# Kernel optimization log

Hardware: AMD Instinct MI355X
Metric: run time of the kernel (lower is better)

The kernel has to match this reference:

```python
import jax, jax.numpy as jnp
import numpy as np

U, I, D, L = 100000, 50000, 64, 2
E_S, E_I = 1200000, 1200000

def spmm(rows, cols, vals, x, num_rows):
    # sparse A (COO) @ dense x : gather source rows, scale, segment-sum into dest rows
    return jax.ops.segment_sum(vals[:, None] * x[cols], rows, num_segments=num_rows)

def setup_inputs() -> dict:
    key = jax.random.key(0)
    ks = jax.random.split(key, 9)
    return {
        "user_emb": jax.random.normal(ks[0], (U, D), jnp.float32) * 0.1,
        "item_emb": jax.random.normal(ks[1], (I, D), jnp.float32) * 0.1,
        "weights": jax.random.normal(ks[2], (L, 2 * D, D), jnp.float32) * (1.0 / np.sqrt(2 * D)),
        "social_vals": jax.random.uniform(ks[3], (E_S,), jnp.float32),
        "inter_vals": jax.random.uniform(ks[4], (E_I,), jnp.float32),
        "social_rows": jax.random.randint(ks[5], (E_S,), 0, U, jnp.int32),
        "social_cols": jax.random.randint(ks[6], (E_S,), 0, U, jnp.int32),
        "inter_rows": jax.random.randint(ks[7], (E_I,), 0, U, jnp.int32),
        "inter_cols": jax.random.randint(ks[8], (E_I,), 0, I, jnp.int32),
    }

def reference(user_emb, item_emb, weights, social_vals, inter_vals,
              social_rows, social_cols, inter_rows, inter_cols):
    u = user_emb
    num_users = user_emb.shape[0]
    for k in range(weights.shape[0]):
        new_u = spmm(social_rows, social_cols, social_vals, u, num_users)  # [U, D]
        u = jnp.concatenate([new_u, u], axis=1) @ weights[k]               # [U, 2D] @ [2D, D]
    final_u = u + spmm(inter_rows, inter_cols, inter_vals, item_emb, num_users)
    return (final_u, item_emb)
```

## Files before the change

### kernel.cpp

```cpp
#include <hip/hip_runtime.h>

#define DD 64
#define RPCB 1024
#define CBSH 10
#define NBLK_P 256

static inline size_t align16(size_t x) { return (x + 15) & ~(size_t)15; }

__device__ __forceinline__ unsigned bf16rn(float f) {
    unsigned u = __float_as_uint(f);
    return (u + 0x7fffu + ((u >> 16) & 1u)) >> 16;
}

typedef __attribute__((ext_vector_type(8))) short bf16x8;
typedef __attribute__((ext_vector_type(4))) float f32x4;

#define VAL_SCALE 32767.0f
#define VAL_INV   (1.0f / 32767.0f)

__global__ __launch_bounds__(1024) void p1_hist(
    const int* __restrict__ srows, const int* __restrict__ irows,
    int* __restrict__ hmat, int ES, int EI, int U, int CB, int EPB)
{
    __shared__ int hist[256];
    const int b = blockIdx.x, t = threadIdx.x;
    for (int i = t; i < CB; i += 1024) hist[i] = 0;
    __syncthreads();
    const int e0 = b * EPB, e1 = min(e0 + EPB, ES + EI);
    for (int e = e0 + t; e < e1; e += 1024) {
        int row = (e < ES) ? srows[e] : U + irows[e - ES];
        atomicAdd(&hist[row >> CBSH], 1);
    }
    __syncthreads();
    for (int i = t; i < CB; i += 1024) hmat[(size_t)i * NBLK_P + b] = hist[i];
}

__global__ __launch_bounds__(256) void scan_partial(
    const int* __restrict__ in, int* __restrict__ out, int* __restrict__ bsums, int n)
{
    __shared__ int sh[256];
    int base = blockIdx.x * 2048 + threadIdx.x * 8;
    int v[8];
    int tsum = 0;
    #pragma unroll
    for (int j = 0; j < 8; ++j) {
        int idx = base + j;
        int x = (idx < n) ? in[idx] : 0;
        v[j] = tsum;
        tsum += x;
    }
    sh[threadIdx.x] = tsum;
    __syncthreads();
    for (int off = 1; off < 256; off <<= 1) {
        int t = (threadIdx.x >= off) ? sh[threadIdx.x - off] : 0;
        __syncthreads();
        sh[threadIdx.x] += t;
        __syncthreads();
    }
    int texc = sh[threadIdx.x] - tsum;
    #pragma unroll
    for (int j = 0; j < 8; ++j) {
        int idx = base + j;
        if (idx < n) out[idx] = texc + v[j];
    }
    if (threadIdx.x == 255) bsums[blockIdx.x] = sh[255];
}

__global__ void scan_top(int* bsums, int nb)
{
    int run = 0;
    for (int i = 0; i < nb; ++i) { int t = bsums[i]; bsums[i] = run; run += t; }
}

__global__ __launch_bounds__(256) void scan_add(
    int* __restrict__ out, const int* __restrict__ bsums, int n)
{
    int i = blockIdx.x * 256 + threadIdx.x;
    if (i < n) out[i] += bsums[i >> 11];
}

__global__ __launch_bounds__(1024) void p2_scatter(
    const int* __restrict__ srows, const int* __restrict__ scols, const float* __restrict__ svals,
    const int* __restrict__ irows, const int* __restrict__ icols, const float* __restrict__ ivals,
    const int* __restrict__ hS, uint2* __restrict__ bedges,
    int ES, int EI, int U, int CB, int EPB)
{
    __shared__ int cur[256];
    const int b = blockIdx.x, t = threadIdx.x;
    for (int i = t; i < CB; i += 1024) cur[i] = hS[(size_t)i * NBLK_P + b];
    __syncthreads();
    const int e0 = b * EPB, e1 = min(e0 + EPB, ES + EI);
    for (int e = e0 + t; e < e1; e += 1024) {
        int row, col; float val;
        if (e < ES) { row = srows[e]; col = scols[e]; val = svals[e]; }
        else {
            int i = e - ES;
            row = U + irows[i]; col = icols[i]; val = ivals[i];
        }
        unsigned q = (unsigned)(val * VAL_SCALE + 0.5f);
        int slot = atomicAdd(&cur[row >> CBSH], 1);
        bedges[slot] = make_uint2(((unsigned)(row & (RPCB - 1)) << 17) | (unsigned)col,
                                  (unsigned)col | (q << 17));
    }
}

__global__ __launch_bounds__(256) void p3_fin(
    const uint2* __restrict__ bedges, const int* __restrict__ hS,
    int* __restrict__ row_ptr, unsigned* __restrict__ edges,
    int n2, int Etot, int CB)
{
    __shared__ int cnt[RPCB];
    __shared__ int sh[256];
    const int cb = blockIdx.x, t = threadIdx.x;
    const int r0 = cb << CBSH;
    const int s = hS[(size_t)cb * NBLK_P];
    const int e = (cb == CB - 1) ? Etot : hS[(size_t)(cb + 1) * NBLK_P];

    #pragma unroll
    for (int j = 0; j < RPCB / 256; ++j) cnt[t + j * 256] = 0;
    __syncthreads();
    for (int i = s + t; i < e; i += 256) atomicAdd(&cnt[bedges[i].x >> 17], 1);
    __syncthreads();

    int c[4]; int tot = 0;
    #pragma unroll
    for (int j = 0; j < 4; ++j) { int x = cnt[t * 4 + j]; c[j] = tot; tot += x; }
    sh[t] = tot;
    __syncthreads();
    for (int off = 1; off < 256; off <<= 1) {
        int v = (t >= off) ? sh[t - off] : 0;
        __syncthreads();
        sh[t] += v;
        __syncthreads();
    }
    int excl = sh[t] - tot;
    #pragma unroll
    for (int j = 0; j < 4; ++j) {
        int r = t * 4 + j;
        int v = s + excl + c[j];
        cnt[r] = v;
        int gr = r0 + r;
        if (gr < n2) row_ptr[gr] = v;
    }
    if (cb == CB - 1 && t == 0) row_ptr[n2] = Etot;
    __syncthreads();

    for (int i = s + t; i < e; i += 256) {
        uint2 ev = bedges[i];
        int r = ev.x >> 17;
        int slot = atomicAdd(&cnt[r], 1);
        edges[slot] = ev.y;
    }
}

__global__ __launch_bounds__(256) void conv_quant(
    const float* __restrict__ uemb, ushort* __restrict__ ubf,
    unsigned char* __restrict__ uq8, float* __restrict__ uscale, int U,
    const float* __restrict__ iemb, unsigned char* __restrict__ iq8,
    float* __restrict__ iscale, float* __restrict__ passI, int I)
{
    int row  = (blockIdx.x * 256 + threadIdx.x) >> 3;
    int lane = threadIdx.x & 7;
    bool isU = (row < U);
    int lrow = isU ? row : row - U;
    if (!isU && lrow >= I) return;
    const float* src = (isU ? uemb : iemb) + ((size_t)lrow << 6) + lane * 8;
    float4 A = *reinterpret_cast<const float4*>(src);
    float4 B = *reinterpret_cast<const float4*>(src + 4);
    float m = fmaxf(fmaxf(fmaxf(fabsf(A.x), fabsf(A.y)), fmaxf(fabsf(A.z), fabsf(A.w))),
                    fmaxf(fmaxf(fabsf(B.x), fabsf(B.y)), fmaxf(fabsf(B.z), fabsf(B.w))));
    m = fmaxf(m, __shfl_xor(m, 1, 8));
    m = fmaxf(m, __shfl_xor(m, 2, 8));
    m = fmaxf(m, __shfl_xor(m, 4, 8));
    float inv = (m > 1e-30f) ? 127.0f / m : 0.0f;
    float sc  = m / 127.0f;
    unsigned b0 = (unsigned)(__float2int_rn(A.x * inv) + 128);
    unsigned b1 = (unsigned)(__float2int_rn(A.y * inv) + 128);
    unsigned b2 = (unsigned)(__float2int_rn(A.z * inv) + 128);
    unsigned b3 = (unsigned)(__float2int_rn(A.w * inv) + 128);
    unsigned b4 = (unsigned)(__float2int_rn(B.x * inv) + 128);
    unsigned b5 = (unsigned)(__float2int_rn(B.y * inv) + 128);
    unsigned b6 = (unsigned)(__float2int_rn(B.z * inv) + 128);
    unsigned b7 = (unsigned)(__float2int_rn(B.w * inv) + 128);
    uint2 pk = make_uint2(b0 | (b1 << 8) | (b2 << 16) | (b3 << 24),
                          b4 | (b5 << 8) | (b6 << 16) | (b7 << 24));
    if (isU) {
        reinterpret_cast<uint2*>(uq8 + ((size_t)lrow << 6) + lane * 8)[0] = pk;
        if (lane == 0) uscale[lrow] = sc;
        uint4 r;
        r.x = bf16rn(A.x) | (bf16rn(A.y) << 16);
        r.y = bf16rn(A.z) | (bf16rn(A.w) << 16);
        r.z = bf16rn(B.x) | (bf16rn(B.y) << 16);
        r.w = bf16rn(B.z) | (bf16rn(B.w) << 16);
        *reinterpret_cast<uint4*>(ubf + ((size_t)lrow << 6) + lane * 8) = r;
    } else {
        reinterpret_cast<uint2*>(iq8 + ((size_t)lrow << 6) + lane * 8)[0] = pk;
        if (lane == 0) iscale[lrow] = sc;
        float* q = passI + ((size_t)lrow << 6) + lane * 8;
        *reinterpret_cast<float4*>(q)     = A;
        *reinterpret_cast<float4*>(q + 4) = B;
    }
}

__global__ __launch_bounds__(256) void rows_to_i8(
    const ushort* __restrict__ bf, unsigned char* __restrict__ q8,
    float* __restrict__ scale, int nrows)
{
    int row  = (blockIdx.x * 256 + threadIdx.x) >> 3;
    int lane = threadIdx.x & 7;
    if (row >= nrows) return;
    uint4 x = *reinterpret_cast<const uint4*>(bf + ((size_t)row << 6) + lane * 8);
    float v0 = __uint_as_float(x.x << 16), v1 = __uint_as_float(x.x & 0xffff0000u);
    float v2 = __uint_as_float(x.y << 16), v3 = __uint_as_float(x.y & 0xffff0000u);
    float v4 = __uint_as_float(x.z << 16), v5 = __uint_as_float(x.z & 0xffff0000u);
    float v6 = __uint_as_float(x.w << 16), v7 = __uint_as_float(x.w & 0xffff0000u);
    float m = fmaxf(fmaxf(fmaxf(fabsf(v0), fabsf(v1)), fmaxf(fabsf(v2), fabsf(v3))),
                    fmaxf(fmaxf(fabsf(v4), fabsf(v5)), fmaxf(fabsf(v6), fabsf(v7))));
    m = fmaxf(m, __shfl_xor(m, 1, 8));
    m = fmaxf(m, __shfl_xor(m, 2, 8));
    m = fmaxf(m, __shfl_xor(m, 4, 8));
    float inv = (m > 1e-30f) ? 127.0f / m : 0.0f;
    unsigned b0 = (unsigned)(__float2int_rn(v0 * inv) + 128);
    unsigned b1 = (unsigned)(__float2int_rn(v1 * inv) + 128);
    unsigned b2 = (unsigned)(__float2int_rn(v2 * inv) + 128);
    unsigned b3 = (unsigned)(__float2int_rn(v3 * inv) + 128);
    unsigned b4 = (unsigned)(__float2int_rn(v4 * inv) + 128);
    unsigned b5 = (unsigned)(__float2int_rn(v5 * inv) + 128);
    unsigned b6 = (unsigned)(__float2int_rn(v6 * inv) + 128);
    unsigned b7 = (unsigned)(__float2int_rn(v7 * inv) + 128);
    uint2 pk = make_uint2(b0 | (b1 << 8) | (b2 << 16) | (b3 << 24),
                          b4 | (b5 << 8) | (b6 << 16) | (b7 << 24));
    reinterpret_cast<uint2*>(q8 + ((size_t)row << 6) + lane * 8)[0] = pk;
    if (lane == 0) scale[row] = m / 127.0f;
}

__global__ __launch_bounds__(256) void conv_w(
    const float* __restrict__ w, ushort* __restrict__ wtb, int n)
{
    int idx = blockIdx.x * 256 + threadIdx.x;
    if (idx >= n) return;
    int l = idx >> 13;
    int r = idx & 8191;
    int c = r >> 7;
    int k = r & 127;
    wtb[idx] = (ushort)bf16rn(w[(size_t)l * 8192 + k * 64 + c]);
}

__device__ __forceinline__ void fma_i8(float4& a0, float4& a1, float& ssum, float veff, uint2 x)
{
    ssum += veff;
    a0.x += veff * (float)(x.x & 0xffu);
    a0.y += veff * (float)((x.x >> 8) & 0xffu);
    a0.z += veff * (float)((x.x >> 16) & 0xffu);
    a0.w += veff * (float)(x.x >> 24);
    a1.x += veff * (float)(x.y & 0xffu);
    a1.y += veff * (float)((x.y >> 8) & 0xffu);
    a1.z += veff * (float)((x.y >> 16) & 0xffu);
    a1.w += veff * (float)(x.y >> 24);
}

template <int MODE>
__global__ __launch_bounds__(256) void spmm_i8(
    const int* __restrict__ row_ptr, const unsigned* __restrict__ edges,
    const unsigned char* __restrict__ q8,
    const float* __restrict__ scalef,
    ushort* __restrict__ outb, float* __restrict__ outf, int nrows)
{
    int g    = (blockIdx.x * 256 + threadIdx.x) >> 3;
    int lane = threadIdx.x & 7;
    if (g >= nrows) return;
    int s = row_ptr[g], e = row_ptr[g + 1];
    float4 a0 = make_float4(0.f, 0.f, 0.f, 0.f);
    float4 a1 = make_float4(0.f, 0.f, 0.f, 0.f);
    float ssum = 0.f;
    int i = s;
    for (; i + 3 < e; i += 4) {
        unsigned e0 = edges[i], e1 = edges[i + 1], e2 = edges[i + 2], e3 = edges[i + 3];
        unsigned c0 = e0 & 0x1FFFFu, c1 = e1 & 0x1FFFFu, c2 = e2 & 0x1FFFFu, c3 = e3 & 0x1FFFFu;
        uint2 x0 = *reinterpret_cast<const uint2*>(q8 + ((size_t)c0 << 6) + lane * 8);
        uint2 x1 = *reinterpret_cast<const uint2*>(q8 + ((size_t)c1 << 6) + lane * 8);
        uint2 x2 = *reinterpret_cast<const uint2*>(q8 + ((size_t)c2 << 6) + lane * 8);
        uint2 x3 = *reinterpret_cast<const uint2*>(q8 + ((size_t)c3 << 6) + lane * 8);
        float v0 = (float)(e0 >> 17) * VAL_INV * scalef[c0];
        float v1 = (float)(e1 >> 17) * VAL_INV * scalef[c1];
        float v2 = (float)(e2 >> 17) * VAL_INV * scalef[c2];
        float v3 = (float)(e3 >> 17) * VAL_INV * scalef[c3];
        fma_i8(a0, a1, ssum, v0, x0);
        fma_i8(a0, a1, ssum, v1, x1);
        fma_i8(a0, a1, ssum, v2, x2);
        fma_i8(a0, a1, ssum, v3, x3);
    }
    for (; i < e; ++i) {
        unsigned e0 = edges[i];
        unsigned c0 = e0 & 0x1FFFFu;
        uint2 x0 = *reinterpret_cast<const uint2*>(q8 + ((size_t)c0 << 6) + lane * 8);
        float v0 = (float)(e0 >> 17) * VAL_INV * scalef[c0];
        fma_i8(a0, a1, ssum, v0, x0);
    }
    float bias = 128.f * ssum;
    a0.x -= bias; a0.y -= bias; a0.z -= bias; a0.w -= bias;
    a1.x -= bias; a1.y -= bias; a1.z -= bias; a1.w -= bias;
    if (MODE == 0) {
        uint4 pk;
        pk.x = bf16rn(a0.x) | (bf16rn(a0.y) << 16);
        pk.y = bf16rn(a0.z) | (bf16rn(a0.w) << 16);
        pk.z = bf16rn(a1.x) | (bf16rn(a1.y) << 16);
        pk.w = bf16rn(a1.z) | (bf16rn(a1.w) << 16);
        *reinterpret_cast<uint4*>(outb + ((size_t)g << 6) + lane * 8) = pk;
    } else {
        float* o = outf + ((size_t)g << 6) + lane * 8;
        float4 c0 = *reinterpret_cast<const float4*>(o);
        float4 c1 = *reinterpret_cast<const float4*>(o + 4);
        a0.x += c0.x; a0.y += c0.y; a0.z += c0.z; a0.w += c0.w;
        a1.x += c1.x; a1.y += c1.y; a1.z += c1.z; a1.w += c1.w;
        *reinterpret_cast<float4*>(o)     = a0;
        *reinterpret_cast<float4*>(o + 4) = a1;
    }
}

template<bool FINAL>
__global__ __launch_bounds__(256) void gemm_mfma(
    const ushort* __restrict__ abf,
    const ushort* __restrict__ bbf,
    const ushort* __restrict__ wtb,
    float* __restrict__ outf,
    ushort* __restrict__ outb,
    int U)
{
    __shared__ ushort sWt[64 * 128];
    const int t = threadIdx.x;

    for (int i = t; i < 1024; i += 256) {
        int c = i >> 4, g = i & 15;
        uint4 v = *reinterpret_cast<const uint4*>(wtb + (size_t)c * 128 + g * 8);
        int gp = g ^ (c & 7);
        *reinterpret_cast<uint4*>(&sWt[c * 128 + gp * 8]) = v;
    }
    __syncthreads();

    const int w    = t >> 6;
    const int l    = t & 63;
    const int l16  = l & 15;
    const int ksub = l >> 4;
    const int grow_base = blockIdx.x * 64 + w * 16;

    const int arow = min(grow_base + l16, U - 1);

    f32x4 acc[4] = {f32x4{0,0,0,0}, f32x4{0,0,0,0}, f32x4{0,0,0,0}, f32x4{0,0,0,0}};

    #pragma unroll
    for (int kk = 0; kk < 4; ++kk) {
        const int kof = kk * 32 + ksub * 8;
        const ushort* asrc = (kk < 2) ? (abf + ((size_t)arow << 6) + kof)
                                      : (bbf + ((size_t)arow << 6) + (kof - 64));
        bf16x8 afrag = *reinterpret_cast<const bf16x8*>(asrc);
        #pragma unroll
        for (int ct = 0; ct < 4; ++ct) {
            int c  = ct * 16 + l16;
            int g  = kk * 4 + ksub;
            int gp = g ^ (c & 7);
            bf16x8 bfrag = *reinterpret_cast<const bf16x8*>(&sWt[c * 128 + gp * 8]);
            acc[ct] = __builtin_amdgcn_mfma_f32_16x16x32_bf16(afrag, bfrag, acc[ct], 0, 0, 0);
        }
    }

    #pragma unroll
    for (int ct = 0; ct < 4; ++ct) {
        #pragma unroll
        for (int j = 0; j < 4; ++j) {
            int grow = grow_base + ksub * 4 + j;
            int gcol = ct * 16 + l16;
            if (grow < U) {
                float v = acc[ct][j];
                if (FINAL) outf[((size_t)grow << 6) + gcol] = v;
                else       outb[((size_t)grow << 6) + gcol] = (ushort)bf16rn(v);
            }
        }
    }
}

extern "C" void kernel_launch(void* const* d_in, const int* in_sizes, int n_in,
                              void* d_out, int out_size, void* d_ws, size_t ws_size,
                              hipStream_t stream)
{
    const float* user_emb    = (const float*)d_in[0];
    const float* item_emb    = (const float*)d_in[1];
    const float* weights     = (const float*)d_in[2];
    const float* social_vals = (const float*)d_in[3];
    const float* inter_vals  = (const float*)d_in[4];
    const int*   social_rows = (const int*)d_in[5];
    const int*   social_cols = (const int*)d_in[6];
    const int*   inter_rows  = (const int*)d_in[7];
    const int*   inter_cols  = (const int*)d_in[8];

    const int D  = DD;
    const int U  = in_sizes[0] / D;
    const int I  = in_sizes[1] / D;
    const int L  = in_sizes[2] / (2 * D * D);
    const int ES = in_sizes[3];
    const int EI = in_sizes[4];

    float* out      = (float*)d_out;
    float* out_item = out + (size_t)U * D;

    char* p = (char*)d_ws;
    size_t off = 0;
    auto take = [&](size_t bytes) { char* r = p + off; off += align16(bytes); return r; };

    const int n2   = 2 * U;
    const int CB   = (n2 + RPCB - 1) >> CBSH;
    const int Etot = ES + EI;
    const int EPB  = (Etot + NBLK_P - 1) / NBLK_P;
    const int NH   = CB * NBLK_P;

    int*           row_ptr = (int*)take((size_t)(n2 + 1) * sizeof(int));
    int*           hmat    = (int*)take((size_t)NH * sizeof(int));
    int*           hS      = (int*)take((size_t)NH * sizeof(int));
    int*           bsums   = (int*)take(1024 * sizeof(int));
    unsigned*      edges   = (unsigned*)take((size_t)Etot * sizeof(unsigned));
    uint2*         bedges  = (uint2*)take((size_t)Etot * sizeof(uint2));
    ushort*        ubf     = (ushort*)take((size_t)U * D * sizeof(ushort));
    unsigned char* uq8     = (unsigned char*)take((size_t)U * D);
    float*         uscale  = (float*)take((size_t)U * sizeof(float));
    unsigned char* iq8     = (unsigned char*)take((size_t)I * D);
    float*         iscale  = (float*)take((size_t)I * sizeof(float));
    ushort*        wtb     = (ushort*)take((size_t)L * 2 * D * D * sizeof(ushort));
    ushort*        tmpA_bf = (ushort*)take((size_t)U * D * sizeof(ushort));
    ushort*        uB_bf   = (ushort*)take((size_t)U * D * sizeof(ushort));
    ushort*        uC_bf   = (ushort*)take((size_t)U * D * sizeof(ushort));
    unsigned char* uB_q8   = (unsigned char*)take((size_t)U * D);
    unsigned char* uC_q8   = (unsigned char*)take((size_t)U * D);
    float*         uB_sc   = (float*)take((size_t)U * sizeof(float));
    float*         uC_sc   = (float*)take((size_t)U * sizeof(float));

    p1_hist<<<NBLK_P, 1024, 0, stream>>>(social_rows, inter_rows, hmat, ES, EI, U, CB, EPB);
    const int nb = (NH + 2047) / 2048;
    scan_partial<<<nb, 256, 0, stream>>>(hmat, hS, bsums, NH);
    scan_top<<<1, 1, 0, stream>>>(bsums, nb);
    scan_add<<<(NH + 255) / 256, 256, 0, stream>>>(hS, bsums, NH);
    p2_scatter<<<NBLK_P, 1024, 0, stream>>>(
        social_rows, social_cols, social_vals,
        inter_rows, inter_cols, inter_vals,
        hS, bedges, ES, EI, U, CB, EPB);
    p3_fin<<<CB, 256, 0, stream>>>(bedges, hS, row_ptr, edges, n2, Etot, CB);

    const int convthreads = (U + I) * 8;
    conv_quant<<<(convthreads + 255) / 256, 256, 0, stream>>>(
        user_emb, ubf, uq8, uscale, U, item_emb, iq8, iscale, out_item, I);
    const int nw = L * 2 * D * D;
    conv_w<<<(nw + 255) / 256, 256, 0, stream>>>(weights, wtb, nw);

    const int spmm_grid = ((U * 8) + 255) / 256;
    const int gemm_grid = (U + 63) / 64;
    const ushort*        uprev_bf = ubf;
    const unsigned char* uprev_q8 = uq8;
    const float*         uprev_sc = uscale;
    int which = 0;
    for (int k = 0; k < L; ++k) {
        const ushort* wk = wtb + (size_t)k * 2 * D * D;
        spmm_i8<0><<<spmm_grid, 256, 0, stream>>>(
            row_ptr, edges, uprev_q8, uprev_sc, tmpA_bf, (float*)nullptr, U);
        if (k == L - 1) {
            gemm_mfma<true><<<gemm_grid, 256, 0, stream>>>(
                tmpA_bf, uprev_bf, wk, out, (ushort*)nullptr, U);
        } else {
            ushort*        nbf = which ? uC_bf : uB_bf;
            unsigned char* nq8 = which ? uC_q8 : uB_q8;
            float*         nsc = which ? uC_sc : uB_sc;
            gemm_mfma<false><<<gemm_grid, 256, 0, stream>>>(
                tmpA_bf, uprev_bf, wk, (float*)nullptr, nbf, U);
            rows_to_i8<<<spmm_grid, 256, 0, stream>>>(nbf, nq8, nsc, U);
            uprev_bf = nbf;
            uprev_q8 = nq8;
            uprev_sc = nsc;
            which ^= 1;
        }
    }

    spmm_i8<1><<<spmm_grid, 256, 0, stream>>>(
        row_ptr + U, edges, iq8, iscale, (ushort*)nullptr, out, U);
}
```

Baseline: 186.7 us.

## Fuse CSR build into cooperative kernel, merge conversions, fold int8 quantization into GEMM

Replaces the six-kernel CSR construction (histogram, three-stage scan, scatter, finalize) with a single cooperative kernel that uses grid-wide syncs between phases. The embedding and weight conversion kernels are merged into one launch. The int8 row quantization that ran as a separate pass after the intermediate GEMM now happens in that GEMM's epilogue through shared memory. The goal is to cut launch overhead and an extra round trip through global memory, at the cost of grid.sync barriers and the constraint that all 256 blocks of 1024 threads must be co-resident.

```diff
diff --git a/kernel.cpp b/kernel.cpp
--- a/kernel.cpp
+++ b/kernel.cpp
@@ -1,4 +1,7 @@
 #include <hip/hip_runtime.h>
+#include <hip/hip_cooperative_groups.h>
+
+namespace cg = cooperative_groups;
 
 #define DD 64
 #define RPCB 1024
@@ -18,232 +21,184 @@
 #define VAL_SCALE 32767.0f
 #define VAL_INV   (1.0f / 32767.0f)
 
-__global__ __launch_bounds__(1024) void p1_hist(
-    const int* __restrict__ srows, const int* __restrict__ irows,
-    int* __restrict__ hmat, int ES, int EI, int U, int CB, int EPB)
-{
-    __shared__ int hist[256];
+__global__ __launch_bounds__(1024) void build_csr_coop(
+    const int* __restrict__ srows, const int* __restrict__ scols, const float* __restrict__ svals,
+    const int* __restrict__ irows, const int* __restrict__ icols, const float* __restrict__ ivals,
+    int* __restrict__ hmat,
+    int* __restrict__ btot,
+    uint2* __restrict__ bedges,
+    int* __restrict__ row_ptr, unsigned* __restrict__ edges,
+    int ES, int EI, int U, int n2, int CB, int EPB)
+{
+    cg::grid_group grid = cg::this_grid();
     const int b = blockIdx.x, t = threadIdx.x;
-    for (int i = t; i < CB; i += 1024) hist[i] = 0;
+    const int Etot = ES + EI;
+    __shared__ int sh[1024];
+    __shared__ int sh2[256];
+
+    for (int i = t; i < CB; i += 1024) sh[i] = 0;
     __syncthreads();
-    const int e0 = b * EPB, e1 = min(e0 + EPB, ES + EI);
+    const int e0 = b * EPB, e1 = min(e0 + EPB, Etot);
     for (int e = e0 + t; e < e1; e += 1024) {
         int row = (e < ES) ? srows[e] : U + irows[e - ES];
-        atomicAdd(&hist[row >> CBSH], 1);
+        atomicAdd(&sh[row >> CBSH], 1);
     }
     __syncthreads();
-    for (int i = t; i < CB; i += 1024) hmat[(size_t)i * NBLK_P + b] = hist[i];
-}
-
-__global__ __launch_bounds__(256) void scan_partial(
-    const int* __restrict__ in, int* __restrict__ out, int* __restrict__ bsums, int n)
-{
-    __shared__ int sh[256];
-    int base = blockIdx.x * 2048 + threadIdx.x * 8;
-    int v[8];
-    int tsum = 0;
-    #pragma unroll
-    for (int j = 0; j < 8; ++j) {
-        int idx = base + j;
-        int x = (idx < n) ? in[idx] : 0;
-        v[j] = tsum;
-        tsum += x;
-    }
-    sh[threadIdx.x] = tsum;
+    for (int i = t; i < CB; i += 1024) hmat[(size_t)i * NBLK_P + b] = sh[i];
+    __threadfence();
+    grid.sync();
+
+    if (b < CB) {
+        int part = 0;
+        for (int i = t; i < NBLK_P; i += 1024) part += hmat[(size_t)b * NBLK_P + i];
+        sh[t] = part;
+        __syncthreads();
+        for (int off = 512; off > 0; off >>= 1) {
+            if (t < off) sh[t] += sh[t + off];
+            __syncthreads();
+        }
+        if (t == 0) btot[b] = sh[0];
+    }
+    __threadfence();
+    grid.sync();
+
+    if (b == 0) {
+        int v = (t < CB) ? btot[t] : 0;
+        if (t < 256) sh[t] = v;
+        __syncthreads();
+        for (int off = 1; off < 256; off <<= 1) {
+            int u2 = (t >= off && t < 256) ? sh[t - off] : 0;
+            __syncthreads();
+            if (t < 256) sh[t] += u2;
+            __syncthreads();
+        }
+        if (t < CB) btot[t] = sh[t] - v;
+    }
+    __threadfence();
+    grid.sync();
+
+    if (b < CB) {
+        int base = btot[b];
+        int v = (t < NBLK_P) ? hmat[(size_t)b * NBLK_P + t] : 0;
+        if (t < 256) sh[t] = v;
+        __syncthreads();
+        for (int off = 1; off < NBLK_P; off <<= 1) {
+            int u2 = (t >= off && t < 256) ? sh[t - off] : 0;
+            __syncthreads();
+            if (t < 256) sh[t] += u2;
+            __syncthreads();
+        }
+        if (t < NBLK_P) hmat[(size_t)b * NBLK_P + t] = base + sh[t] - v;
+    }
+    __threadfence();
+    grid.sync();
+
+    for (int i = t; i < CB; i += 1024) sh2[i] = hmat[(size_t)i * NBLK_P + b];
     __syncthreads();
-    for (int off = 1; off < 256; off <<= 1) {
-        int t = (threadIdx.x >= off) ? sh[threadIdx.x - off] : 0;
-        __syncthreads();
-        sh[threadIdx.x] += t;
-        __syncthreads();
-    }
-    int texc = sh[threadIdx.x] - tsum;
-    #pragma unroll
-    for (int j = 0; j < 8; ++j) {
-        int idx = base + j;
-        if (idx < n) out[idx] = texc + v[j];
-    }
-    if (threadIdx.x == 255) bsums[blockIdx.x] = sh[255];
-}
-
-__global__ void scan_top(int* bsums, int nb)
-{
-    int run = 0;
-    for (int i = 0; i < nb; ++i) { int t = bsums[i]; bsums[i] = run; run += t; }
-}
-
-__global__ __launch_bounds__(256) void scan_add(
-    int* __restrict__ out, const int* __restrict__ bsums, int n)
-{
-    int i = blockIdx.x * 256 + threadIdx.x;
-    if (i < n) out[i] += bsums[i >> 11];
-}
-
-__global__ __launch_bounds__(1024) void p2_scatter(
-    const int* __restrict__ srows, const int* __restrict__ scols, const float* __restrict__ svals,
-    const int* __restrict__ irows, const int* __restrict__ icols, const float* __restrict__ ivals,
-    const int* __restrict__ hS, uint2* __restrict__ bedges,
-    int ES, int EI, int U, int CB, int EPB)
-{
-    __shared__ int cur[256];
-    const int b = blockIdx.x, t = threadIdx.x;
-    for (int i = t; i < CB; i += 1024) cur[i] = hS[(size_t)i * NBLK_P + b];
-    __syncthreads();
-    const int e0 = b * EPB, e1 = min(e0 + EPB, ES + EI);
     for (int e = e0 + t; e < e1; e += 1024) {
         int row, col; float val;
         if (e < ES) { row = srows[e]; col = scols[e]; val = svals[e]; }
-        else {
-            int i = e - ES;
-            row = U + irows[i]; col = icols[i]; val = ivals[i];
-        }
+        else { int i = e - ES; row = U + irows[i]; col = icols[i]; val = ivals[i]; }
         unsigned q = (unsigned)(val * VAL_SCALE + 0.5f);
-        int slot = atomicAdd(&cur[row >> CBSH], 1);
+        int slot = atomicAdd(&sh2[row >> CBSH], 1);
         bedges[slot] = make_uint2(((unsigned)(row & (RPCB - 1)) << 17) | (unsigned)col,
                                   (unsigned)col | (q << 17));
     }
-}
-
-__global__ __launch_bounds__(256) void p3_fin(
-    const uint2* __restrict__ bedges, const int* __restrict__ hS,
-    int* __restrict__ row_ptr, unsigned* __restrict__ edges,
-    int n2, int Etot, int CB)
-{
-    __shared__ int cnt[RPCB];
-    __shared__ int sh[256];
-    const int cb = blockIdx.x, t = threadIdx.x;
-    const int r0 = cb << CBSH;
-    const int s = hS[(size_t)cb * NBLK_P];
-    const int e = (cb == CB - 1) ? Etot : hS[(size_t)(cb + 1) * NBLK_P];
-
-    #pragma unroll
-    for (int j = 0; j < RPCB / 256; ++j) cnt[t + j * 256] = 0;
-    __syncthreads();
-    for (int i = s + t; i < e; i += 256) atomicAdd(&cnt[bedges[i].x >> 17], 1);
-    __syncthreads();
-
-    int c[4]; int tot = 0;
-    #pragma unroll
-    for (int j = 0; j < 4; ++j) { int x = cnt[t * 4 + j]; c[j] = tot; tot += x; }
-    sh[t] = tot;
-    __syncthreads();
-    for (int off = 1; off < 256; off <<= 1) {
-        int v = (t >= off) ? sh[t - off] : 0;
-        __syncthreads();
-        sh[t] += v;
-        __syncthreads();
-    }
-    int excl = sh[t] - tot;
-    #pragma unroll
-    for (int j = 0; j < 4; ++j) {
-        int r = t * 4 + j;
-        int v = s + excl + c[j];
-        cnt[r] = v;
-        int gr = r0 + r;
+    __threadfence();
+    grid.sync();
+
+    if (b < CB) {
+        const int r0 = b << CBSH;
+        const int s = hmat[(size_t)b * NBLK_P];
+        const int e = (b == CB - 1) ? Etot : hmat[(size_t)(b + 1) * NBLK_P];
+        sh[t] = 0;
+        __syncthreads();
+        for (int i = s + t; i < e; i += 1024) atomicAdd(&sh[bedges[i].x >> 17], 1);
+        __syncthreads();
+        int c = sh[t];
+        __syncthreads();
+        sh[t] = c;
+        __syncthreads();
+        for (int off = 1; off < 1024; off <<= 1) {
+            int u2 = (t >= off) ? sh[t - off] : 0;
+            __syncthreads();
+            sh[t] += u2;
+            __syncthreads();
+        }
+        int v = s + sh[t] - c;
+        __syncthreads();
+        sh[t] = v;
+        int gr = r0 + t;
         if (gr < n2) row_ptr[gr] = v;
-    }
-    if (cb == CB - 1 && t == 0) row_ptr[n2] = Etot;
-    __syncthreads();
-
-    for (int i = s + t; i < e; i += 256) {
-        uint2 ev = bedges[i];
-        int r = ev.x >> 17;
-        int slot = atomicAdd(&cnt[r], 1);
-        edges[slot] = ev.y;
-    }
-}
-
-__global__ __launch_bounds__(256) void conv_quant(
+        if (b == CB - 1 && t == 0) row_ptr[n2] = Etot;
+        __syncthreads();
+        for (int i = s + t; i < e; i += 1024) {
+            uint2 ev = bedges[i];
+            int slot = atomicAdd(&sh[ev.x >> 17], 1);
+            edges[slot] = ev.y;
+        }
+    }
+}
+
+__global__ __launch_bounds__(256) void conv_all(
     const float* __restrict__ uemb, ushort* __restrict__ ubf,
     unsigned char* __restrict__ uq8, float* __restrict__ uscale, int U,
     const float* __restrict__ iemb, unsigned char* __restrict__ iq8,
-    float* __restrict__ iscale, float* __restrict__ passI, int I)
-{
-    int row  = (blockIdx.x * 256 + threadIdx.x) >> 3;
-    int lane = threadIdx.x & 7;
-    bool isU = (row < U);
-    int lrow = isU ? row : row - U;
-    if (!isU && lrow >= I) return;
-    const float* src = (isU ? uemb : iemb) + ((size_t)lrow << 6) + lane * 8;
-    float4 A = *reinterpret_cast<const float4*>(src);
-    float4 B = *reinterpret_cast<const float4*>(src + 4);
-    float m = fmaxf(fmaxf(fmaxf(fabsf(A.x), fabsf(A.y)), fmaxf(fabsf(A.z), fabsf(A.w))),
-                    fmaxf(fmaxf(fabsf(B.x), fabsf(B.y)), fmaxf(fabsf(B.z), fabsf(B.w))));
-    m = fmaxf(m, __shfl_xor(m, 1, 8));
-    m = fmaxf(m, __shfl_xor(m, 2, 8));
-    m = fmaxf(m, __shfl_xor(m, 4, 8));
-    float inv = (m > 1e-30f) ? 127.0f / m : 0.0f;
-    float sc  = m / 127.0f;
-    unsigned b0 = (unsigned)(__float2int_rn(A.x * inv) + 128);
-    unsigned b1 = (unsigned)(__float2int_rn(A.y * inv) + 128);
-    unsigned b2 = (unsigned)(__float2int_rn(A.z * inv) + 128);
-    unsigned b3 = (unsigned)(__float2int_rn(A.w * inv) + 128);
-    unsigned b4 = (unsigned)(__float2int_rn(B.x * inv) + 128);
-    unsigned b5 = (unsigned)(__float2int_rn(B.y * inv) + 128);
-    unsigned b6 = (unsigned)(__float2int_rn(B.z * inv) + 128);
-    unsigned b7 = (unsigned)(__float2int_rn(B.w * inv) + 128);
-    uint2 pk = make_uint2(b0 | (b1 << 8) | (b2 << 16) | (b3 << 24),
-                          b4 | (b5 << 8) | (b6 << 16) | (b7 << 24));
-    if (isU) {
-        reinterpret_cast<uint2*>(uq8 + ((size_t)lrow << 6) + lane * 8)[0] = pk;
-        if (lane == 0) uscale[lrow] = sc;
-        uint4 r;
-        r.x = bf16rn(A.x) | (bf16rn(A.y) << 16);
-        r.y = bf16rn(A.z) | (bf16rn(A.w) << 16);
-        r.z = bf16rn(B.x) | (bf16rn(B.y) << 16);
-        r.w = bf16rn(B.z) | (bf16rn(B.w) << 16);
-        *reinterpret_cast<uint4*>(ubf + ((size_t)lrow << 6) + lane * 8) = r;
+    float* __restrict__ iscale, float* __restrict__ passI, int I,
+    const float* __restrict__ w, ushort* __restrict__ wtb, int nw)
+{
+    int idx = blockIdx.x * 256 + threadIdx.x;
+    const int qthreads = (U + I) * 8;
+    if (idx < qthreads) {
+        int row  = idx >> 3;
+        int lane = idx & 7;
+        bool isU = (row < U);
+        int lrow = isU ? row : row - U;
+        const float* src = (isU ? uemb : iemb) + ((size_t)lrow << 6) + lane * 8;
+        float4 A = *reinterpret_cast<const float4*>(src);
+        float4 B = *reinterpret_cast<const float4*>(src + 4);
+        float m = fmaxf(fmaxf(fmaxf(fabsf(A.x), fabsf(A.y)), fmaxf(fabsf(A.z), fabsf(A.w))),
+                        fmaxf(fmaxf(fabsf(B.x), fabsf(B.y)), fmaxf(fabsf(B.z), fabsf(B.w))));
+        m = fmaxf(m, __shfl_xor(m, 1, 8));
+        m = fmaxf(m, __shfl_xor(m, 2, 8));
+        m = fmaxf(m, __shfl_xor(m, 4, 8));
+        float inv = (m > 1e-30f) ? 127.0f / m : 0.0f;
+        unsigned b0 = (unsigned)(__float2int_rn(A.x * inv) + 128);
+        unsigned b1 = (unsigned)(__float2int_rn(A.y * inv) + 128);
+        unsigned b2 = (unsigned)(__float2int_rn(A.z * inv) + 128);
+        unsigned b3 = (unsigned)(__float2int_rn(A.w * inv) + 128);
+        unsigned b4 = (unsigned)(__float2int_rn(B.x * inv) + 128);
+        unsigned b5 = (unsigned)(__float2int_rn(B.y * inv) + 128);
+        unsigned b6 = (unsigned)(__float2int_rn(B.z * inv) + 128);
+        unsigned b7 = (unsigned)(__float2int_rn(B.w * inv) + 128);
+        uint2 pk = make_uint2(b0 | (b1 << 8) | (b2 << 16) | (b3 << 24),
+                              b4 | (b5 << 8) | (b6 << 16) | (b7 << 24));
+        if (isU) {
+            reinterpret_cast<uint2*>(uq8 + ((size_t)lrow << 6) + lane * 8)[0] = pk;
+            if (lane == 0) uscale[lrow] = m / 127.0f;
+            uint4 r;
+            r.x = bf16rn(A.x) | (bf16rn(A.y) << 16);
+            r.y = bf16rn(A.z) | (bf16rn(A.w) << 16);
+            r.z = bf16rn(B.x) | (bf16rn(B.y) << 16);
+            r.w = bf16rn(B.z) | (bf16rn(B.w) << 16);
+            *reinterpret_cast<uint4*>(ubf + ((size_t)lrow << 6) + lane * 8) = r;
+        } else {
+            reinterpret_cast<uint2*>(iq8 + ((size_t)lrow << 6) + lane * 8)[0] = pk;
+            if (lane == 0) iscale[lrow] = m / 127.0f;
+            float* q = passI + ((size_t)lrow << 6) + lane * 8;
+            *reinterpret_cast<float4*>(q)     = A;
+            *reinterpret_cast<float4*>(q + 4) = B;
+        }
     } else {
-        reinterpret_cast<uint2*>(iq8 + ((size_t)lrow << 6) + lane * 8)[0] = pk;
-        if (lane == 0) iscale[lrow] = sc;
-        float* q = passI + ((size_t)lrow << 6) + lane * 8;
-        *reinterpret_cast<float4*>(q)     = A;
-        *reinterpret_cast<float4*>(q + 4) = B;
-    }
-}
-
-__global__ __launch_bounds__(256) void rows_to_i8(
-    const ushort* __restrict__ bf, unsigned char* __restrict__ q8,
-    float* __restrict__ scale, int nrows)
-{
-    int row  = (blockIdx.x * 256 + threadIdx.x) >> 3;
-    int lane = threadIdx.x & 7;
-    if (row >= nrows) return;
-    uint4 x = *reinterpret_cast<const uint4*>(bf + ((size_t)row << 6) + lane * 8);
-    float v0 = __uint_as_float(x.x << 16), v1 = __uint_as_float(x.x & 0xffff0000u);
-    float v2 = __uint_as_float(x.y << 16), v3 = __uint_as_float(x.y & 0xffff0000u);
-    float v4 = __uint_as_float(x.z << 16), v5 = __uint_as_float(x.z & 0xffff0000u);
-    float v6 = __uint_as_float(x.w << 16), v7 = __uint_as_float(x.w & 0xffff0000u);
-    float m = fmaxf(fmaxf(fmaxf(fabsf(v0), fabsf(v1)), fmaxf(fabsf(v2), fabsf(v3))),
-                    fmaxf(fmaxf(fabsf(v4), fabsf(v5)), fmaxf(fabsf(v6), fabsf(v7))));
-    m = fmaxf(m, __shfl_xor(m, 1, 8));
-    m = fmaxf(m, __shfl_xor(m, 2, 8));
-    m = fmaxf(m, __shfl_xor(m, 4, 8));
-    float inv = (m > 1e-30f) ? 127.0f / m : 0.0f;
-    unsigned b0 = (unsigned)(__float2int_rn(v0 * inv) + 128);
-    unsigned b1 = (unsigned)(__float2int_rn(v1 * inv) + 128);
-    unsigned b2 = (unsigned)(__float2int_rn(v2 * inv) + 128);
-    unsigned b3 = (unsigned)(__float2int_rn(v3 * inv) + 128);
-    unsigned b4 = (unsigned)(__float2int_rn(v4 * inv) + 128);
-    unsigned b5 = (unsigned)(__float2int_rn(v5 * inv) + 128);
-    unsigned b6 = (unsigned)(__float2int_rn(v6 * inv) + 128);
-    unsigned b7 = (unsigned)(__float2int_rn(v7 * inv) + 128);
-    uint2 pk = make_uint2(b0 | (b1 << 8) | (b2 << 16) | (b3 << 24),
-                          b4 | (b5 << 8) | (b6 << 16) | (b7 << 24));
-    reinterpret_cast<uint2*>(q8 + ((size_t)row << 6) + lane * 8)[0] = pk;
-    if (lane == 0) scale[row] = m / 127.0f;
-}
-
-__global__ __launch_bounds__(256) void conv_w(
-    const float* __restrict__ w, ushort* __restrict__ wtb, int n)
-{
-    int idx = blockIdx.x * 256 + threadIdx.x;
-    if (idx >= n) return;
-    int l = idx >> 13;
-    int r = idx & 8191;
-    int c = r >> 7;
-    int k = r & 127;
-    wtb[idx] = (ushort)bf16rn(w[(size_t)l * 8192 + k * 64 + c]);
+        int widx = idx - qthreads;
+        if (widx < nw) {
+            int l = widx >> 13;
+            int r = widx & 8191;
+            int c = r >> 7;
+            int k = r & 127;
+            wtb[widx] = (ushort)bf16rn(w[(size_t)l * 8192 + k * 64 + c]);
+        }
+    }
 }
 
 __device__ __forceinline__ void fma_i8(float4& a0, float4& a1, float& ssum, float veff, uint2 x)
@@ -325,6 +280,8 @@
     const ushort* __restrict__ wtb,
     float* __restrict__ outf,
     ushort* __restrict__ outb,
+    unsigned char* __restrict__ q8,
+    float* __restrict__ scale,
     int U)
 {
     __shared__ ushort sWt[64 * 128];
@@ -343,7 +300,6 @@
     const int l16  = l & 15;
     const int ksub = l >> 4;
     const int grow_base = blockIdx.x * 64 + w * 16;
-
     const int arow = min(grow_base + l16, U - 1);
 
     f32x4 acc[4] = {f32x4{0,0,0,0}, f32x4{0,0,0,0}, f32x4{0,0,0,0}, f32x4{0,0,0,0}};
@@ -364,16 +320,59 @@
         }
     }
 
-    #pragma unroll
-    for (int ct = 0; ct < 4; ++ct) {
+    if (FINAL) {
         #pragma unroll
-        for (int j = 0; j < 4; ++j) {
-            int grow = grow_base + ksub * 4 + j;
-            int gcol = ct * 16 + l16;
+        for (int ct = 0; ct < 4; ++ct) {
+            #pragma unroll
+            for (int j = 0; j < 4; ++j) {
+                int grow = grow_base + ksub * 4 + j;
+                int gcol = ct * 16 + l16;
+                if (grow < U) outf[((size_t)grow << 6) + gcol] = acc[ct][j];
+            }
+        }
+    } else {
+        __syncthreads();
+        ushort* sOut = sWt;
+        #pragma unroll
+        for (int ct = 0; ct < 4; ++ct) {
+            #pragma unroll
+            for (int j = 0; j < 4; ++j) {
+                int rloc = w * 16 + ksub * 4 + j;
+                int col  = ct * 16 + l16;
+                sOut[rloc * 72 + col] = (ushort)bf16rn(acc[ct][j]);
+            }
+        }
+        __syncthreads();
+        #pragma unroll
+        for (int pass = 0; pass < 2; ++pass) {
+            int rloc = pass * 32 + (t >> 3);
+            int lane = t & 7;
+            int grow = blockIdx.x * 64 + rloc;
+            uint4 x = *reinterpret_cast<const uint4*>(&sOut[rloc * 72 + lane * 8]);
+            float v0 = __uint_as_float(x.x << 16), v1 = __uint_as_float(x.x & 0xffff0000u);
+            float v2 = __uint_as_float(x.y << 16), v3 = __uint_as_float(x.y & 0xffff0000u);
+            float v4 = __uint_as_float(x.z << 16), v5 = __uint_as_float(x.z & 0xffff0000u);
+            float v6 = __uint_as_float(x.w << 16), v7 = __uint_as_float(x.w & 0xffff0000u);
+            float m = fmaxf(fmaxf(fmaxf(fabsf(v0), fabsf(v1)), fmaxf(fabsf(v2), fabsf(v3))),
+                            fmaxf(fmaxf(fabsf(v4), fabsf(v5)), fmaxf(fabsf(v6), fabsf(v7))));
+            m = fmaxf(m, __shfl_xor(m, 1, 8));
+            m = fmaxf(m, __shfl_xor(m, 2, 8));
+            m = fmaxf(m, __shfl_xor(m, 4, 8));
+            float inv = (m > 1e-30f) ? 127.0f / m : 0.0f;
+            unsigned b0 = (unsigned)(__float2int_rn(v0 * inv) + 128);
+            unsigned b1 = (unsigned)(__float2int_rn(v1 * inv) + 128);
+            unsigned b2 = (unsigned)(__float2int_rn(v2 * inv) + 128);
+            unsigned b3 = (unsigned)(__float2int_rn(v3 * inv) + 128);
+            unsigned b4 = (unsigned)(__float2int_rn(v4 * inv) + 128);
+            unsigned b5 = (unsigned)(__float2int_rn(v5 * inv) + 128);
+            unsigned b6 = (unsigned)(__float2int_rn(v6 * inv) + 128);
+            unsigned b7 = (unsigned)(__float2int_rn(v7 * inv) + 128);
+            uint2 pk = make_uint2(b0 | (b1 << 8) | (b2 << 16) | (b3 << 24),
+                                  b4 | (b5 << 8) | (b6 << 16) | (b7 << 24));
             if (grow < U) {
-                float v = acc[ct][j];
-                if (FINAL) outf[((size_t)grow << 6) + gcol] = v;
-                else       outb[((size_t)grow << 6) + gcol] = (ushort)bf16rn(v);
+                *reinterpret_cast<uint4*>(outb + ((size_t)grow << 6) + lane * 8) = x;
+                reinterpret_cast<uint2*>(q8 + ((size_t)grow << 6) + lane * 8)[0] = pk;
+                if (lane == 0) scale[grow] = m / 127.0f;
             }
         }
     }
@@ -415,8 +414,7 @@
 
     int*           row_ptr = (int*)take((size_t)(n2 + 1) * sizeof(int));
     int*           hmat    = (int*)take((size_t)NH * sizeof(int));
-    int*           hS      = (int*)take((size_t)NH * sizeof(int));
-    int*           bsums   = (int*)take(1024 * sizeof(int));
+    int*           btot    = (int*)take(256 * sizeof(int));
     unsigned*      edges   = (unsigned*)take((size_t)Etot * sizeof(unsigned));
     uint2*         bedges  = (uint2*)take((size_t)Etot * sizeof(uint2));
     ushort*        ubf     = (ushort*)take((size_t)U * D * sizeof(ushort));
@@ -433,22 +431,23 @@
     float*         uB_sc   = (float*)take((size_t)U * sizeof(float));
     float*         uC_sc   = (float*)take((size_t)U * sizeof(float));
 
-    p1_hist<<<NBLK_P, 1024, 0, stream>>>(social_rows, inter_rows, hmat, ES, EI, U, CB, EPB);
-    const int nb = (NH + 2047) / 2048;
-    scan_partial<<<nb, 256, 0, stream>>>(hmat, hS, bsums, NH);
-    scan_top<<<1, 1, 0, stream>>>(bsums, nb);
-    scan_add<<<(NH + 255) / 256, 256, 0, stream>>>(hS, bsums, NH);
-    p2_scatter<<<NBLK_P, 1024, 0, stream>>>(
-        social_rows, social_cols, social_vals,
-        inter_rows, inter_cols, inter_vals,
-        hS, bedges, ES, EI, U, CB, EPB);
-    p3_fin<<<CB, 256, 0, stream>>>(bedges, hS, row_ptr, edges, n2, Etot, CB);
-
-    const int convthreads = (U + I) * 8;
-    conv_quant<<<(convthreads + 255) / 256, 256, 0, stream>>>(
-        user_emb, ubf, uq8, uscale, U, item_emb, iq8, iscale, out_item, I);
+    {
+        int ES_ = ES, EI_ = EI, U_ = U, n2_ = n2, CB_ = CB, EPB_ = EPB;
+        void* args[] = {
+            (void*)&social_rows, (void*)&social_cols, (void*)&social_vals,
+            (void*)&inter_rows, (void*)&inter_cols, (void*)&inter_vals,
+            (void*)&hmat, (void*)&btot, (void*)&bedges, (void*)&row_ptr, (void*)&edges,
+            (void*)&ES_, (void*)&EI_, (void*)&U_, (void*)&n2_, (void*)&CB_, (void*)&EPB_
+        };
+        hipLaunchCooperativeKernel((void*)build_csr_coop, dim3(NBLK_P), dim3(1024),
+                                   args, 0, stream);
+    }
+
     const int nw = L * 2 * D * D;
-    conv_w<<<(nw + 255) / 256, 256, 0, stream>>>(weights, wtb, nw);
+    const int convthreads = (U + I) * 8 + nw;
+    conv_all<<<(convthreads + 255) / 256, 256, 0, stream>>>(
+        user_emb, ubf, uq8, uscale, U, item_emb, iq8, iscale, out_item, I,
+        weights, wtb, nw);
 
     const int spmm_grid = ((U * 8) + 255) / 256;
     const int gemm_grid = (U + 63) / 64;
@@ -462,14 +461,14 @@
             row_ptr, edges, uprev_q8, uprev_sc, tmpA_bf, (float*)nullptr, U);
         if (k == L - 1) {
             gemm_mfma<true><<<gemm_grid, 256, 0, stream>>>(
-                tmpA_bf, uprev_bf, wk, out, (ushort*)nullptr, U);
+                tmpA_bf, uprev_bf, wk, out, (ushort*)nullptr,
+                (unsigned char*)nullptr, (float*)nullptr, U);
         } else {
             ushort*        nbf = which ? uC_bf : uB_bf;
             unsigned char* nq8 = which ? uC_q8 : uB_q8;
             float*         nsc = which ? uC_sc : uB_sc;
             gemm_mfma<false><<<gemm_grid, 256, 0, stream>>>(
-                tmpA_bf, uprev_bf, wk, (float*)nullptr, nbf, U);
-            rows_to_i8<<<spmm_grid, 256, 0, stream>>>(nbf, nq8, nsc, U);
+                tmpA_bf, uprev_bf, wk, (float*)nullptr, nbf, nq8, nsc, U);
             uprev_bf = nbf;
             uprev_q8 = nq8;
             uprev_sc = nsc;
```

Result: slower. 694.7 us (+272.0%).

## Fuse int8 requantization into GEMM epilogue and merge conversion kernels

Applied to the files above, without the earlier changes.

The non-final GEMM now stages its bf16 output tile in shared memory, then computes each row's int8 quantization and scale in the epilogue. It writes bf16, q8 and scale together with vectorized stores, which removes the separate rows_to_i8 kernel and its re-read of the bf16 buffer. The input quantization and weight-conversion kernels are merged into one launch to cut launch overhead. The cost is extra shared-memory traffic and two block barriers in the GEMM epilogue.

```diff
diff --git a/kernel.cpp b/kernel.cpp
--- a/kernel.cpp
+++ b/kernel.cpp
@@ -153,97 +153,65 @@
     }
 }
 
-__global__ __launch_bounds__(256) void conv_quant(
+__global__ __launch_bounds__(256) void conv_all(
     const float* __restrict__ uemb, ushort* __restrict__ ubf,
     unsigned char* __restrict__ uq8, float* __restrict__ uscale, int U,
     const float* __restrict__ iemb, unsigned char* __restrict__ iq8,
-    float* __restrict__ iscale, float* __restrict__ passI, int I)
-{
-    int row  = (blockIdx.x * 256 + threadIdx.x) >> 3;
-    int lane = threadIdx.x & 7;
-    bool isU = (row < U);
-    int lrow = isU ? row : row - U;
-    if (!isU && lrow >= I) return;
-    const float* src = (isU ? uemb : iemb) + ((size_t)lrow << 6) + lane * 8;
-    float4 A = *reinterpret_cast<const float4*>(src);
-    float4 B = *reinterpret_cast<const float4*>(src + 4);
-    float m = fmaxf(fmaxf(fmaxf(fabsf(A.x), fabsf(A.y)), fmaxf(fabsf(A.z), fabsf(A.w))),
-                    fmaxf(fmaxf(fabsf(B.x), fabsf(B.y)), fmaxf(fabsf(B.z), fabsf(B.w))));
-    m = fmaxf(m, __shfl_xor(m, 1, 8));
-    m = fmaxf(m, __shfl_xor(m, 2, 8));
-    m = fmaxf(m, __shfl_xor(m, 4, 8));
-    float inv = (m > 1e-30f) ? 127.0f / m : 0.0f;
-    float sc  = m / 127.0f;
-    unsigned b0 = (unsigned)(__float2int_rn(A.x * inv) + 128);
-    unsigned b1 = (unsigned)(__float2int_rn(A.y * inv) + 128);
-    unsigned b2 = (unsigned)(__float2int_rn(A.z * inv) + 128);
-    unsigned b3 = (unsigned)(__float2int_rn(A.w * inv) + 128);
-    unsigned b4 = (unsigned)(__float2int_rn(B.x * inv) + 128);
-    unsigned b5 = (unsigned)(__float2int_rn(B.y * inv) + 128);
-    unsigned b6 = (unsigned)(__float2int_rn(B.z * inv) + 128);
-    unsigned b7 = (unsigned)(__float2int_rn(B.w * inv) + 128);
-    uint2 pk = make_uint2(b0 | (b1 << 8) | (b2 << 16) | (b3 << 24),
-                          b4 | (b5 << 8) | (b6 << 16) | (b7 << 24));
-    if (isU) {
-        reinterpret_cast<uint2*>(uq8 + ((size_t)lrow << 6) + lane * 8)[0] = pk;
-        if (lane == 0) uscale[lrow] = sc;
-        uint4 r;
-        r.x = bf16rn(A.x) | (bf16rn(A.y) << 16);
-        r.y = bf16rn(A.z) | (bf16rn(A.w) << 16);
-        r.z = bf16rn(B.x) | (bf16rn(B.y) << 16);
-        r.w = bf16rn(B.z) | (bf16rn(B.w) << 16);
-        *reinterpret_cast<uint4*>(ubf + ((size_t)lrow << 6) + lane * 8) = r;
+    float* __restrict__ iscale, float* __restrict__ passI, int I,
+    const float* __restrict__ w, ushort* __restrict__ wtb, int nw)
+{
+    int idx = blockIdx.x * 256 + threadIdx.x;
+    const int qthreads = (U + I) * 8;
+    if (idx < qthreads) {
+        int row  = idx >> 3;
+        int lane = idx & 7;
+        bool isU = (row < U);
+        int lrow = isU ? row : row - U;
+        const float* src = (isU ? uemb : iemb) + ((size_t)lrow << 6) + lane * 8;
+        float4 A = *reinterpret_cast<const float4*>(src);
+        float4 B = *reinterpret_cast<const float4*>(src + 4);
+        float m = fmaxf(fmaxf(fmaxf(fabsf(A.x), fabsf(A.y)), fmaxf(fabsf(A.z), fabsf(A.w))),
+                        fmaxf(fmaxf(fabsf(B.x), fabsf(B.y)), fmaxf(fabsf(B.z), fabsf(B.w))));
+        m = fmaxf(m, __shfl_xor(m, 1, 8));
+        m = fmaxf(m, __shfl_xor(m, 2, 8));
+        m = fmaxf(m, __shfl_xor(m, 4, 8));
+        float inv = (m > 1e-30f) ? 127.0f / m : 0.0f;
+        unsigned b0 = (unsigned)(__float2int_rn(A.x * inv) + 128);
+        unsigned b1 = (unsigned)(__float2int_rn(A.y * inv) + 128);
+        unsigned b2 = (unsigned)(__float2int_rn(A.z * inv) + 128);
+        unsigned b3 = (unsigned)(__float2int_rn(A.w * inv) + 128);
+        unsigned b4 = (unsigned)(__float2int_rn(B.x * inv) + 128);
+        unsigned b5 = (unsigned)(__float2int_rn(B.y * inv) + 128);
+        unsigned b6 = (unsigned)(__float2int_rn(B.z * inv) + 128);
+        unsigned b7 = (unsigned)(__float2int_rn(B.w * inv) + 128);
+        uint2 pk = make_uint2(b0 | (b1 << 8) | (b2 << 16) | (b3 << 24),
+                              b4 | (b5 << 8) | (b6 << 16) | (b7 << 24));
+        if (isU) {
+            reinterpret_cast<uint2*>(uq8 + ((size_t)lrow << 6) + lane * 8)[0] = pk;
+            if (lane == 0) uscale[lrow] = m / 127.0f;
+            uint4 r;
+            r.x = bf16rn(A.x) | (bf16rn(A.y) << 16);
+            r.y = bf16rn(A.z) | (bf16rn(A.w) << 16);
+            r.z = bf16rn(B.x) | (bf16rn(B.y) << 16);
+            r.w = bf16rn(B.z) | (bf16rn(B.w) << 16);
+            *reinterpret_cast<uint4*>(ubf + ((size_t)lrow << 6) + lane * 8) = r;
+        } else {
+            reinterpret_cast<uint2*>(iq8 + ((size_t)lrow << 6) + lane * 8)[0] = pk;
+            if (lane == 0) iscale[lrow] = m / 127.0f;
+            float* q = passI + ((size_t)lrow << 6) + lane * 8;
+            *reinterpret_cast<float4*>(q)     = A;
+            *reinterpret_cast<float4*>(q + 4) = B;
+        }
     } else {
-        reinterpret_cast<uint2*>(iq8 + ((size_t)lrow << 6) + lane * 8)[0] = pk;
-        if (lane == 0) iscale[lrow] = sc;
-        float* q = passI + ((size_t)lrow << 6) + lane * 8;
-        *reinterpret_cast<float4*>(q)     = A;
-        *reinterpret_cast<float4*>(q + 4) = B;
-    }
-}
-
-__global__ __launch_bounds__(256) void rows_to_i8(
-    const ushort* __restrict__ bf, unsigned char* __restrict__ q8,
-    float* __restrict__ scale, int nrows)
-{
-    int row  = (blockIdx.x * 256 + threadIdx.x) >> 3;
-    int lane = threadIdx.x & 7;
-    if (row >= nrows) return;
-    uint4 x = *reinterpret_cast<const uint4*>(bf + ((size_t)row << 6) + lane * 8);
-    float v0 = __uint_as_float(x.x << 16), v1 = __uint_as_float(x.x & 0xffff0000u);
-    float v2 = __uint_as_float(x.y << 16), v3 = __uint_as_float(x.y & 0xffff0000u);
-    float v4 = __uint_as_float(x.z << 16), v5 = __uint_as_float(x.z & 0xffff0000u);
-    float v6 = __uint_as_float(x.w << 16), v7 = __uint_as_float(x.w & 0xffff0000u);
-    float m = fmaxf(fmaxf(fmaxf(fabsf(v0), fabsf(v1)), fmaxf(fabsf(v2), fabsf(v3))),
-                    fmaxf(fmaxf(fabsf(v4), fabsf(v5)), fmaxf(fabsf(v6), fabsf(v7))));
-    m = fmaxf(m, __shfl_xor(m, 1, 8));
-    m = fmaxf(m, __shfl_xor(m, 2, 8));
-    m = fmaxf(m, __shfl_xor(m, 4, 8));
-    float inv = (m > 1e-30f) ? 127.0f / m : 0.0f;
-    unsigned b0 = (unsigned)(__float2int_rn(v0 * inv) + 128);
-    unsigned b1 = (unsigned)(__float2int_rn(v1 * inv) + 128);
-    unsigned b2 = (unsigned)(__float2int_rn(v2 * inv) + 128);
-    unsigned b3 = (unsigned)(__float2int_rn(v3 * inv) + 128);
-    unsigned b4 = (unsigned)(__float2int_rn(v4 * inv) + 128);
-    unsigned b5 = (unsigned)(__float2int_rn(v5 * inv) + 128);
-    unsigned b6 = (unsigned)(__float2int_rn(v6 * inv) + 128);
-    unsigned b7 = (unsigned)(__float2int_rn(v7 * inv) + 128);
-    uint2 pk = make_uint2(b0 | (b1 << 8) | (b2 << 16) | (b3 << 24),
-                          b4 | (b5 << 8) | (b6 << 16) | (b7 << 24));
-    reinterpret_cast<uint2*>(q8 + ((size_t)row << 6) + lane * 8)[0] = pk;
-    if (lane == 0) scale[row] = m / 127.0f;
-}
-
-__global__ __launch_bounds__(256) void conv_w(
-    const float* __restrict__ w, ushort* __restrict__ wtb, int n)
-{
-    int idx = blockIdx.x * 256 + threadIdx.x;
-    if (idx >= n) return;
-    int l = idx >> 13;
-    int r = idx & 8191;
-    int c = r >> 7;
-    int k = r & 127;
-    wtb[idx] = (ushort)bf16rn(w[(size_t)l * 8192 + k * 64 + c]);
+        int widx = idx - qthreads;
+        if (widx < nw) {
+            int l = widx >> 13;
+            int r = widx & 8191;
+            int c = r >> 7;
+            int k = r & 127;
+            wtb[widx] = (ushort)bf16rn(w[(size_t)l * 8192 + k * 64 + c]);
+        }
+    }
 }
 
 __device__ __forceinline__ void fma_i8(float4& a0, float4& a1, float& ssum, float veff, uint2 x)
@@ -325,6 +293,8 @@
     const ushort* __restrict__ wtb,
     float* __restrict__ outf,
     ushort* __restrict__ outb,
+    unsigned char* __restrict__ q8,
+    float* __restrict__ scale,
     int U)
 {
     __shared__ ushort sWt[64 * 128];
@@ -343,7 +313,6 @@
     const int l16  = l & 15;
     const int ksub = l >> 4;
     const int grow_base = blockIdx.x * 64 + w * 16;
-
     const int arow = min(grow_base + l16, U - 1);
 
     f32x4 acc[4] = {f32x4{0,0,0,0}, f32x4{0,0,0,0}, f32x4{0,0,0,0}, f32x4{0,0,0,0}};
@@ -364,16 +333,59 @@
         }
     }
 
-    #pragma unroll
-    for (int ct = 0; ct < 4; ++ct) {
+    if (FINAL) {
         #pragma unroll
-        for (int j = 0; j < 4; ++j) {
-            int grow = grow_base + ksub * 4 + j;
-            int gcol = ct * 16 + l16;
+        for (int ct = 0; ct < 4; ++ct) {
+            #pragma unroll
+            for (int j = 0; j < 4; ++j) {
+                int grow = grow_base + ksub * 4 + j;
+                int gcol = ct * 16 + l16;
+                if (grow < U) outf[((size_t)grow << 6) + gcol] = acc[ct][j];
+            }
+        }
+    } else {
+        __syncthreads();
+        ushort* sOut = sWt;
+        #pragma unroll
+        for (int ct = 0; ct < 4; ++ct) {
+            #pragma unroll
+            for (int j = 0; j < 4; ++j) {
+                int rloc = w * 16 + ksub * 4 + j;
+                int col  = ct * 16 + l16;
+                sOut[rloc * 72 + col] = (ushort)bf16rn(acc[ct][j]);
+            }
+        }
+        __syncthreads();
+        #pragma unroll
+        for (int pass = 0; pass < 2; ++pass) {
+            int rloc = pass * 32 + (t >> 3);
+            int lane = t & 7;
+            int grow = blockIdx.x * 64 + rloc;
+            uint4 x = *reinterpret_cast<const uint4*>(&sOut[rloc * 72 + lane * 8]);
+            float v0 = __uint_as_float(x.x << 16), v1 = __uint_as_float(x.x & 0xffff0000u);
+            float v2 = __uint_as_float(x.y << 16), v3 = __uint_as_float(x.y & 0xffff0000u);
+            float v4 = __uint_as_float(x.z << 16), v5 = __uint_as_float(x.z & 0xffff0000u);
+            float v6 = __uint_as_float(x.w << 16), v7 = __uint_as_float(x.w & 0xffff0000u);
+            float m = fmaxf(fmaxf(fmaxf(fabsf(v0), fabsf(v1)), fmaxf(fabsf(v2), fabsf(v3))),
+                            fmaxf(fmaxf(fabsf(v4), fabsf(v5)), fmaxf(fabsf(v6), fabsf(v7))));
+            m = fmaxf(m, __shfl_xor(m, 1, 8));
+            m = fmaxf(m, __shfl_xor(m, 2, 8));
+            m = fmaxf(m, __shfl_xor(m, 4, 8));
+            float inv = (m > 1e-30f) ? 127.0f / m : 0.0f;
+            unsigned b0 = (unsigned)(__float2int_rn(v0 * inv) + 128);
+            unsigned b1 = (unsigned)(__float2int_rn(v1 * inv) + 128);
+            unsigned b2 = (unsigned)(__float2int_rn(v2 * inv) + 128);
+            unsigned b3 = (unsigned)(__float2int_rn(v3 * inv) + 128);
+            unsigned b4 = (unsigned)(__float2int_rn(v4 * inv) + 128);
+            unsigned b5 = (unsigned)(__float2int_rn(v5 * inv) + 128);
+            unsigned b6 = (unsigned)(__float2int_rn(v6 * inv) + 128);
+            unsigned b7 = (unsigned)(__float2int_rn(v7 * inv) + 128);
+            uint2 pk = make_uint2(b0 | (b1 << 8) | (b2 << 16) | (b3 << 24),
+                                  b4 | (b5 << 8) | (b6 << 16) | (b7 << 24));
             if (grow < U) {
-                float v = acc[ct][j];
-                if (FINAL) outf[((size_t)grow << 6) + gcol] = v;
-                else       outb[((size_t)grow << 6) + gcol] = (ushort)bf16rn(v);
+                *reinterpret_cast<uint4*>(outb + ((size_t)grow << 6) + lane * 8) = x;
+                reinterpret_cast<uint2*>(q8 + ((size_t)grow << 6) + lane * 8)[0] = pk;
+                if (lane == 0) scale[grow] = m / 127.0f;
             }
         }
     }
@@ -444,11 +456,11 @@
         hS, bedges, ES, EI, U, CB, EPB);
     p3_fin<<<CB, 256, 0, stream>>>(bedges, hS, row_ptr, edges, n2, Etot, CB);
 
-    const int convthreads = (U + I) * 8;
-    conv_quant<<<(convthreads + 255) / 256, 256, 0, stream>>>(
-        user_emb, ubf, uq8, uscale, U, item_emb, iq8, iscale, out_item, I);
     const int nw = L * 2 * D * D;
-    conv_w<<<(nw + 255) / 256, 256, 0, stream>>>(weights, wtb, nw);
+    const int convthreads = (U + I) * 8 + nw;
+    conv_all<<<(convthreads + 255) / 256, 256, 0, stream>>>(
+        user_emb, ubf, uq8, uscale, U, item_emb, iq8, iscale, out_item, I,
+        weights, wtb, nw);
 
     const int spmm_grid = ((U * 8) + 255) / 256;
     const int gemm_grid = (U + 63) / 64;
@@ -462,14 +474,14 @@
             row_ptr, edges, uprev_q8, uprev_sc, tmpA_bf, (float*)nullptr, U);
         if (k == L - 1) {
             gemm_mfma<true><<<gemm_grid, 256, 0, stream>>>(
-                tmpA_bf, uprev_bf, wk, out, (ushort*)nullptr, U);
+                tmpA_bf, uprev_bf, wk, out, (ushort*)nullptr,
+                (unsigned char*)nullptr, (float*)nullptr, U);
         } else {
             ushort*        nbf = which ? uC_bf : uB_bf;
             unsigned char* nq8 = which ? uC_q8 : uB_q8;
             float*         nsc = which ? uC_sc : uB_sc;
             gemm_mfma<false><<<gemm_grid, 256, 0, stream>>>(
-                tmpA_bf, uprev_bf, wk, (float*)nullptr, nbf, U);
-            rows_to_i8<<<spmm_grid, 256, 0, stream>>>(nbf, nq8, nsc, U);
+                tmpA_bf, uprev_bf, wk, (float*)nullptr, nbf, nq8, nsc, U);
             uprev_bf = nbf;
             uprev_q8 = nq8;
             uprev_sc = nsc;
```

New measurement: 179.2 us. 1.04x faster.
